# Kernel tuning notes

Hardware: AMD Instinct MI355X
Metric: run time of the kernel (lower is better)

Reference implementation:

```python
import jax, jax.numpy as jnp
import numpy as np

E = 1024
H = 16
DFF = 4 * E
EPS = 1e-5


def layer_norm(x, scale, bias):
    mu = jnp.mean(x, axis=-1, keepdims=True)
    var = jnp.var(x, axis=-1, keepdims=True)
    return (x - mu) * jax.lax.rsqrt(var + EPS) * scale + bias


def setup_inputs() -> dict:
    key = jax.random.key(0)
    ks = jax.random.split(key, 12)
    N, L = 2, 2048
    x = jax.random.normal(ks[0], (N, L, E), dtype=jnp.float32)
    attn_mask = jax.random.randint(ks[1], (N, H, L, L), 0, 2) == 1
    s = 0.02
    return {
        "x": x,
        "attn_mask": attn_mask,
        "ln1_s": jnp.ones((E,), jnp.float32),
        "ln1_b": jnp.zeros((E,), jnp.float32),
        "Wqkv": jax.random.normal(ks[2], (E, 3 * E), jnp.float32) * s,
        "bqkv": jnp.zeros((3 * E,), jnp.float32),
        "Wo": jax.random.normal(ks[3], (E, E), jnp.float32) * s,
        "bo": jnp.zeros((E,), jnp.float32),
        "ln2_s": jnp.ones((E,), jnp.float32),
        "ln2_b": jnp.zeros((E,), jnp.float32),
        "lnf_s": jnp.ones((E,), jnp.float32),
        "lnf_b": jnp.zeros((E,), jnp.float32),
        "W1": jax.random.normal(ks[4], (E, DFF), jnp.float32) * s,
        "b1": jnp.zeros((DFF,), jnp.float32),
        "W2": jax.random.normal(ks[5], (DFF, E), jnp.float32) * s,
        "b2": jnp.zeros((E,), jnp.float32),
    }


def reference(x, attn_mask, ln1_s, ln1_b, Wqkv, bqkv, Wo, bo,
              ln2_s, ln2_b, lnf_s, lnf_b, W1, b1, W2, b2):
    N, L, _ = x.shape
    D = E // H
    # --- self attention (pre-norm) ---
    h = layer_norm(x, ln1_s, ln1_b)
    qkv = h @ Wqkv + bqkv                      # [N,L,3E]
    q, k, v = jnp.split(qkv, 3, axis=-1)
    q = q.reshape(N, L, H, D)
    k = k.reshape(N, L, H, D)
    v = v.reshape(N, L, H, D)
    a = jnp.einsum('nqhd,nkhd->nhqk', q, k) * (D ** -0.5)  # [N,H,L,L]
    a = jnp.where(attn_mask, -jnp.inf, a)
    a = jax.nn.softmax(a, axis=-1)
    o = jnp.einsum('nhqk,nkhd->nqhd', a, v).reshape(N, L, E)
    o = o @ Wo + bo
    x = x + o
    # --- feedforward (norm_2 then FF's internal LN) ---
    h = layer_norm(x, ln2_s, ln2_b)
    h = layer_norm(h, lnf_s, lnf_b)
    h = jax.nn.gelu(h @ W1 + b1, approximate=False) @ W2 + b2
    return x + h
```

## Files before the change

kernel.cpp:

```cpp
#include <hip/hip_runtime.h>
#include <math.h>

#define E_DIM 1024
#define H_HEADS 16
#define D_HEAD 64
#define DFF_DIM 4096
#define L_SEQ 2048
#define N_BATCH 2
#define T_TOK (N_BATCH * L_SEQ)

typedef __attribute__((ext_vector_type(8))) __bf16 bf16x8;
typedef __attribute__((ext_vector_type(4))) float f32x4;

__device__ __forceinline__ unsigned short f2bf(float f) {
  union { float f; unsigned int u; } v; v.f = f;
  unsigned int r = v.u + 0x7fffu + ((v.u >> 16) & 1u);
  return (unsigned short)(r >> 16);
}

__global__ __launch_bounds__(256) void convert_transpose(
    const float* __restrict__ in, unsigned short* __restrict__ out, int K, int N) {
  __shared__ float tile[32][33];
  int n0 = blockIdx.x * 32, k0 = blockIdx.y * 32;
  int tx = threadIdx.x & 31, ty = threadIdx.x >> 5;
#pragma unroll
  for (int i = 0; i < 32; i += 8)
    tile[ty + i][tx] = in[(size_t)(k0 + ty + i) * N + n0 + tx];
  __syncthreads();
#pragma unroll
  for (int i = 0; i < 32; i += 8)
    out[(size_t)(n0 + ty + i) * K + k0 + tx] = f2bf(tile[tx][ty + i]);
}

__device__ __forceinline__ void block_reduce2(float& a, float& b, float* sm, int tid) {
#pragma unroll
  for (int off = 32; off > 0; off >>= 1) {
    a += __shfl_down(a, off);
    b += __shfl_down(b, off);
  }
  int wid = tid >> 6;
  if ((tid & 63) == 0) { sm[wid * 2] = a; sm[wid * 2 + 1] = b; }
  __syncthreads();
  a = sm[0] + sm[2] + sm[4] + sm[6];
  b = sm[1] + sm[3] + sm[5] + sm[7];
}

__global__ __launch_bounds__(256) void ln_kernel(
    const float* __restrict__ x, const float* __restrict__ s,
    const float* __restrict__ b, unsigned short* __restrict__ out) {
  int row = blockIdx.x, tid = threadIdx.x;
  __shared__ float sm[8];
  float4 v = ((const float4*)(x + (size_t)row * E_DIM))[tid];
  float sum = v.x + v.y + v.z + v.w;
  float sq = v.x * v.x + v.y * v.y + v.z * v.z + v.w * v.w;
  block_reduce2(sum, sq, sm, tid);
  float mu = sum * (1.0f / E_DIM);
  float var = sq * (1.0f / E_DIM) - mu * mu;
  float rs = rsqrtf(var + 1e-5f);
  float4 sv = ((const float4*)s)[tid];
  float4 bv = ((const float4*)b)[tid];
  ushort4 o4;
  o4.x = f2bf((v.x - mu) * rs * sv.x + bv.x);
  o4.y = f2bf((v.y - mu) * rs * sv.y + bv.y);
  o4.z = f2bf((v.z - mu) * rs * sv.z + bv.z);
  o4.w = f2bf((v.w - mu) * rs * sv.w + bv.w);
  ((ushort4*)(out + (size_t)row * E_DIM))[tid] = o4;
}

__global__ __launch_bounds__(256) void ln2_kernel(
    const float* __restrict__ x, const float* __restrict__ s2,
    const float* __restrict__ b2, const float* __restrict__ sf,
    const float* __restrict__ bf_, unsigned short* __restrict__ out) {
  int row = blockIdx.x, tid = threadIdx.x;
  __shared__ float sm[8];
  float4 v = ((const float4*)(x + (size_t)row * E_DIM))[tid];
  float sum = v.x + v.y + v.z + v.w;
  float sq = v.x * v.x + v.y * v.y + v.z * v.z + v.w * v.w;
  block_reduce2(sum, sq, sm, tid);
  float mu = sum * (1.0f / E_DIM);
  float rs = rsqrtf(sq * (1.0f / E_DIM) - mu * mu + 1e-5f);
  float4 s2v = ((const float4*)s2)[tid];
  float4 b2v = ((const float4*)b2)[tid];
  float y0 = (v.x - mu) * rs * s2v.x + b2v.x;
  float y1 = (v.y - mu) * rs * s2v.y + b2v.y;
  float y2 = (v.z - mu) * rs * s2v.z + b2v.z;
  float y3 = (v.w - mu) * rs * s2v.w + b2v.w;
  float sum2 = y0 + y1 + y2 + y3;
  float sq2 = y0 * y0 + y1 * y1 + y2 * y2 + y3 * y3;
  __syncthreads();
  block_reduce2(sum2, sq2, sm, tid);
  float mu2 = sum2 * (1.0f / E_DIM);
  float rs2 = rsqrtf(sq2 * (1.0f / E_DIM) - mu2 * mu2 + 1e-5f);
  float4 sfv = ((const float4*)sf)[tid];
  float4 bfv = ((const float4*)bf_)[tid];
  ushort4 o4;
  o4.x = f2bf((y0 - mu2) * rs2 * sfv.x + bfv.x);
  o4.y = f2bf((y1 - mu2) * rs2 * sfv.y + bfv.y);
  o4.z = f2bf((y2 - mu2) * rs2 * sfv.z + bfv.z);
  o4.w = f2bf((y3 - mu2) * rs2 * sfv.w + bfv.w);
  ((ushort4*)(out + (size_t)row * E_DIM))[tid] = o4;
}

template <int EPI>
__global__ __launch_bounds__(256) void gemm_bt(
    const unsigned short* __restrict__ A, const unsigned short* __restrict__ Bt,
    const float* __restrict__ bias, const float* __restrict__ resid,
    void* __restrict__ outp, int M, int N, int K) {
  __shared__ unsigned short As[128 * 40];
  __shared__ unsigned short Bs[128 * 40];
  int tid = threadIdx.x;
  int lane = tid & 63, wave = tid >> 6;
  int m0 = blockIdx.y * 128, n0 = blockIdx.x * 128;
  int wm = (wave & 1) * 64, wn = (wave >> 1) * 64;
  int lm = lane & 15, lq = lane >> 4;
  int trow = tid >> 2, tcol = tid & 3;
  f32x4 acc[4][4] = {};
  for (int k0 = 0; k0 < K; k0 += 32) {
    uint4 av0 = *(const uint4*)(A + (size_t)(m0 + trow) * K + k0 + tcol * 8);
    uint4 av1 = *(const uint4*)(A + (size_t)(m0 + trow + 64) * K + k0 + tcol * 8);
    uint4 bv0 = *(const uint4*)(Bt + (size_t)(n0 + trow) * K + k0 + tcol * 8);
    uint4 bv1 = *(const uint4*)(Bt + (size_t)(n0 + trow + 64) * K + k0 + tcol * 8);
    __syncthreads();
    *(uint4*)(As + trow * 40 + tcol * 8) = av0;
    *(uint4*)(As + (trow + 64) * 40 + tcol * 8) = av1;
    *(uint4*)(Bs + trow * 40 + tcol * 8) = bv0;
    *(uint4*)(Bs + (trow + 64) * 40 + tcol * 8) = bv1;
    __syncthreads();
    bf16x8 a[4], b[4];
#pragma unroll
    for (int i = 0; i < 4; i++)
      a[i] = *(const bf16x8*)(As + (wm + i * 16 + lm) * 40 + lq * 8);
#pragma unroll
    for (int j = 0; j < 4; j++)
      b[j] = *(const bf16x8*)(Bs + (wn + j * 16 + lm) * 40 + lq * 8);
#pragma unroll
    for (int i = 0; i < 4; i++)
#pragma unroll
      for (int j = 0; j < 4; j++)
        acc[i][j] = __builtin_amdgcn_mfma_f32_16x16x32_bf16(a[i], b[j], acc[i][j], 0, 0, 0);
  }
#pragma unroll
  for (int i = 0; i < 4; i++)
#pragma unroll
    for (int j = 0; j < 4; j++) {
      int row = m0 + wm + i * 16 + lq * 4;
      int col = n0 + wn + j * 16 + lm;
      float bcol = bias[col];
#pragma unroll
      for (int r = 0; r < 4; r++) {
        float v = acc[i][j][r] + bcol;
        size_t idx = (size_t)(row + r) * N + col;
        if (EPI == 0) {
          ((unsigned short*)outp)[idx] = f2bf(v);
        } else if (EPI == 1) {
          float g = 0.5f * v * (1.0f + erff(v * 0.70710678118f));
          ((unsigned short*)outp)[idx] = f2bf(g);
        } else {
          ((float*)outp)[idx] = resid[idx] + v;
        }
      }
    }
}

__global__ __launch_bounds__(256) void attn_kernel(
    const unsigned short* __restrict__ qkv, const int* __restrict__ mask,
    unsigned short* __restrict__ o) {
  const int bq = blockIdx.x;
  const int nh = blockIdx.y;
  const int h = nh & 15;
  const int tid = threadIdx.x, lane = tid & 63, wave = tid >> 6;
  const int lm = lane & 15, lq = lane >> 4;

  __shared__ unsigned short Ks[64 * 72];
  __shared__ unsigned short Vs[64 * 66];
  __shared__ unsigned short Ps[4][16 * 72];

  const int q_base = bq * 64;
  const int tok0 = (nh >> 4) * L_SEQ;
  const int qoff = h * 64, koff = E_DIM + h * 64, voff = 2 * E_DIM + h * 64;
  const int* mbase = mask + (size_t)nh * L_SEQ * L_SEQ;

  bf16x8 qf[2];
  {
    int t = tok0 + q_base + wave * 16 + lm;
    const unsigned short* qr = qkv + (size_t)t * (3 * E_DIM) + qoff + lq * 8;
    qf[0] = *(const bf16x8*)(qr);
    qf[1] = *(const bf16x8*)(qr + 32);
  }

  float m_run[4], l_run[4];
  f32x4 oacc[4] = {};
#pragma unroll
  for (int r = 0; r < 4; r++) { m_run[r] = -1e30f; l_run[r] = 0.0f; }

  for (int kt = 0; kt < L_SEQ / 64; kt++) {
    const int k_base = kt * 64;
    __syncthreads();
    {
      int row = tid >> 3, chunk = tid & 7;
#pragma unroll
      for (int it = 0; it < 2; it++) {
        int key = row + it * 32;
        int t = tok0 + k_base + key;
        uint4 kv = *(const uint4*)(qkv + (size_t)t * (3 * E_DIM) + koff + chunk * 8);
        *(uint4*)(Ks + key * 72 + chunk * 8) = kv;
        uint4 vv = *(const uint4*)(qkv + (size_t)t * (3 * E_DIM) + voff + chunk * 8);
        unsigned int* vw = (unsigned int*)(Vs + key * 66 + chunk * 8);
        vw[0] = vv.x; vw[1] = vv.y; vw[2] = vv.z; vw[3] = vv.w;
      }
    }
    __syncthreads();

    f32x4 s[4];
#pragma unroll
    for (int nt = 0; nt < 4; nt++) {
      bf16x8 kb0 = *(const bf16x8*)(Ks + (nt * 16 + lm) * 72 + lq * 8);
      bf16x8 kb1 = *(const bf16x8*)(Ks + (nt * 16 + lm) * 72 + 32 + lq * 8);
      f32x4 acc = {};
      acc = __builtin_amdgcn_mfma_f32_16x16x32_bf16(qf[0], kb0, acc, 0, 0, 0);
      acc = __builtin_amdgcn_mfma_f32_16x16x32_bf16(qf[1], kb1, acc, 0, 0, 0);
      s[nt] = acc;
    }
    const int qrow = q_base + wave * 16 + lq * 4;
#pragma unroll
    for (int nt = 0; nt < 4; nt++) {
      int kcol = k_base + nt * 16 + lm;
#pragma unroll
      for (int r = 0; r < 4; r++) {
        float v = s[nt][r] * 0.125f;
        int mval = mbase[(size_t)(qrow + r) * L_SEQ + kcol];
        s[nt][r] = mval ? -1e30f : v;
      }
    }
    float alpha[4], rsum[4];
#pragma unroll
    for (int r = 0; r < 4; r++) {
      float v = fmaxf(fmaxf(s[0][r], s[1][r]), fmaxf(s[2][r], s[3][r]));
#pragma unroll
      for (int mo = 1; mo < 16; mo <<= 1) v = fmaxf(v, __shfl_xor(v, mo));
      float mn = fmaxf(m_run[r], v);
      alpha[r] = __expf(m_run[r] - mn);
      m_run[r] = mn;
      rsum[r] = 0.0f;
    }
    unsigned short* pw = Ps[wave];
#pragma unroll
    for (int nt = 0; nt < 4; nt++)
#pragma unroll
      for (int r = 0; r < 4; r++) {
        float p = __expf(s[nt][r] - m_run[r]);
        rsum[r] += p;
        pw[(lq * 4 + r) * 72 + nt * 16 + lm] = f2bf(p);
      }
#pragma unroll
    for (int r = 0; r < 4; r++) {
      float v = rsum[r];
#pragma unroll
      for (int mo = 1; mo < 16; mo <<= 1) v += __shfl_xor(v, mo);
      l_run[r] = l_run[r] * alpha[r] + v;
    }
#pragma unroll
    for (int j = 0; j < 4; j++)
#pragma unroll
      for (int r = 0; r < 4; r++) oacc[j][r] *= alpha[r];
    __syncthreads();

#pragma unroll
    for (int c = 0; c < 2; c++) {
      bf16x8 pa = *(const bf16x8*)(pw + lm * 72 + c * 32 + lq * 8);
#pragma unroll
      for (int j = 0; j < 4; j++) {
        bf16x8 vb;
#pragma unroll
        for (int jj = 0; jj < 8; jj++)
          vb[jj] = *(const __bf16*)(Vs + (c * 32 + lq * 8 + jj) * 66 + j * 16 + lm);
        oacc[j] = __builtin_amdgcn_mfma_f32_16x16x32_bf16(pa, vb, oacc[j], 0, 0, 0);
      }
    }
  }
  const int qrow = q_base + wave * 16 + lq * 4;
#pragma unroll
  for (int r = 0; r < 4; r++) {
    float inv_l = 1.0f / l_run[r];
    int t = tok0 + qrow + r;
#pragma unroll
    for (int j = 0; j < 4; j++)
      o[(size_t)t * E_DIM + h * 64 + j * 16 + lm] = f2bf(oacc[j][r] * inv_l);
  }
}

extern "C" void kernel_launch(void* const* d_in, const int* in_sizes, int n_in,
                              void* d_out, int out_size, void* d_ws, size_t ws_size,
                              hipStream_t stream) {
  const float* x = (const float*)d_in[0];
  const int* mask = (const int*)d_in[1];
  const float* ln1_s = (const float*)d_in[2];
  const float* ln1_b = (const float*)d_in[3];
  const float* Wqkv = (const float*)d_in[4];
  const float* bqkv = (const float*)d_in[5];
  const float* Wo = (const float*)d_in[6];
  const float* bo = (const float*)d_in[7];
  const float* ln2_s = (const float*)d_in[8];
  const float* ln2_b = (const float*)d_in[9];
  const float* lnf_s = (const float*)d_in[10];
  const float* lnf_b = (const float*)d_in[11];
  const float* W1 = (const float*)d_in[12];
  const float* b1 = (const float*)d_in[13];
  const float* W2 = (const float*)d_in[14];
  const float* b2 = (const float*)d_in[15];

  size_t off = 0;
  auto alloc = [&](size_t bytes) {
    void* p = (char*)d_ws + off;
    off += (bytes + 255) & ~(size_t)255;
    return p;
  };
  unsigned short* WqkvT = (unsigned short*)alloc((size_t)3072 * 1024 * 2);
  unsigned short* WoT = (unsigned short*)alloc((size_t)1024 * 1024 * 2);
  unsigned short* W1T = (unsigned short*)alloc((size_t)4096 * 1024 * 2);
  unsigned short* W2T = (unsigned short*)alloc((size_t)1024 * 4096 * 2);
  unsigned short* h1 = (unsigned short*)alloc((size_t)T_TOK * E_DIM * 2);
  unsigned short* qkvb = (unsigned short*)alloc((size_t)T_TOK * 3 * E_DIM * 2);
  unsigned short* ob = (unsigned short*)alloc((size_t)T_TOK * E_DIM * 2);
  float* x2 = (float*)alloc((size_t)T_TOK * E_DIM * 4);
  unsigned short* h2 = (unsigned short*)alloc((size_t)T_TOK * E_DIM * 2);
  unsigned short* g1 = (unsigned short*)alloc((size_t)T_TOK * DFF_DIM * 2);

  convert_transpose<<<dim3(3072 / 32, 1024 / 32), 256, 0, stream>>>(Wqkv, WqkvT, 1024, 3072);
  convert_transpose<<<dim3(1024 / 32, 1024 / 32), 256, 0, stream>>>(Wo, WoT, 1024, 1024);
  convert_transpose<<<dim3(4096 / 32, 1024 / 32), 256, 0, stream>>>(W1, W1T, 1024, 4096);
  convert_transpose<<<dim3(1024 / 32, 4096 / 32), 256, 0, stream>>>(W2, W2T, 4096, 1024);
  ln_kernel<<<T_TOK, 256, 0, stream>>>(x, ln1_s, ln1_b, h1);
  gemm_bt<0><<<dim3(3072 / 128, T_TOK / 128), 256, 0, stream>>>(
      h1, WqkvT, bqkv, nullptr, qkvb, T_TOK, 3072, 1024);
  attn_kernel<<<dim3(L_SEQ / 64, N_BATCH * H_HEADS), 256, 0, stream>>>(qkvb, mask, ob);
  gemm_bt<2><<<dim3(1024 / 128, T_TOK / 128), 256, 0, stream>>>(
      ob, WoT, bo, x, x2, T_TOK, 1024, 1024);
  ln2_kernel<<<T_TOK, 256, 0, stream>>>(x2, ln2_s, ln2_b, lnf_s, lnf_b, h2);
  gemm_bt<1><<<dim3(DFF_DIM / 128, T_TOK / 128), 256, 0, stream>>>(
      h2, W1T, b1, nullptr, g1, T_TOK, DFF_DIM, 1024);
  gemm_bt<2><<<dim3(1024 / 128, T_TOK / 128), 256, 0, stream>>>(
      g1, W2T, b2, x2, (float*)d_out, T_TOK, 1024, 4096);

  (void)in_sizes; (void)n_in; (void)out_size; (void)ws_size;
}
```

Before: 1.071 ms.

## Load GEMM tiles directly into LDS and store V transposed with XOR swizzle

The GEMM mainloop now uses global_load_lds to copy A and B tiles straight from global memory into LDS, skipping the register round-trip, and drops the padding from the LDS layout. The attention kernel stores V transposed into LDS with an XOR swizzle, so each PV MFMA operand is fetched with one 16-byte read instead of eight scalar bf16 reads. The unpadded GEMM LDS layout may bring back bank conflicts on fragment reads, and the transposed V store becomes eight scalar LDS writes per chunk.

```diff
diff --git a/kernel.cpp b/kernel.cpp
--- a/kernel.cpp
+++ b/kernel.cpp
@@ -16,6 +16,12 @@
   union { float f; unsigned int u; } v; v.f = f;
   unsigned int r = v.u + 0x7fffu + ((v.u >> 16) & 1u);
   return (unsigned short)(r >> 16);
+}
+
+__device__ __forceinline__ void gld16(const void* g, void* l) {
+  __builtin_amdgcn_global_load_lds(
+      (const __attribute__((address_space(1))) unsigned int*)g,
+      (__attribute__((address_space(3))) unsigned int*)l, 16, 0, 0);
 }
 
 __global__ __launch_bounds__(256) void convert_transpose(
@@ -106,33 +112,34 @@
     const unsigned short* __restrict__ A, const unsigned short* __restrict__ Bt,
     const float* __restrict__ bias, const float* __restrict__ resid,
     void* __restrict__ outp, int M, int N, int K) {
-  __shared__ unsigned short As[128 * 40];
-  __shared__ unsigned short Bs[128 * 40];
+  __shared__ unsigned short As[128 * 32];
+  __shared__ unsigned short Bs[128 * 32];
   int tid = threadIdx.x;
   int lane = tid & 63, wave = tid >> 6;
   int m0 = blockIdx.y * 128, n0 = blockIdx.x * 128;
   int wm = (wave & 1) * 64, wn = (wave >> 1) * 64;
   int lm = lane & 15, lq = lane >> 4;
-  int trow = tid >> 2, tcol = tid & 3;
+  int srow = wave * 32 + (lane >> 2);
+  int scol = (lane & 3) * 8;
+  const unsigned short* Ag = A + (size_t)(m0 + srow) * K + scol;
+  const unsigned short* Bg = Bt + (size_t)(n0 + srow) * K + scol;
+  unsigned short* AsW = As + wave * 1024;
+  unsigned short* BsW = Bs + wave * 1024;
   f32x4 acc[4][4] = {};
   for (int k0 = 0; k0 < K; k0 += 32) {
-    uint4 av0 = *(const uint4*)(A + (size_t)(m0 + trow) * K + k0 + tcol * 8);
-    uint4 av1 = *(const uint4*)(A + (size_t)(m0 + trow + 64) * K + k0 + tcol * 8);
-    uint4 bv0 = *(const uint4*)(Bt + (size_t)(n0 + trow) * K + k0 + tcol * 8);
-    uint4 bv1 = *(const uint4*)(Bt + (size_t)(n0 + trow + 64) * K + k0 + tcol * 8);
-    __syncthreads();
-    *(uint4*)(As + trow * 40 + tcol * 8) = av0;
-    *(uint4*)(As + (trow + 64) * 40 + tcol * 8) = av1;
-    *(uint4*)(Bs + trow * 40 + tcol * 8) = bv0;
-    *(uint4*)(Bs + (trow + 64) * 40 + tcol * 8) = bv1;
+    __syncthreads();
+    gld16(Ag + k0, AsW);
+    gld16(Ag + (size_t)16 * K + k0, AsW + 512);
+    gld16(Bg + k0, BsW);
+    gld16(Bg + (size_t)16 * K + k0, BsW + 512);
     __syncthreads();
     bf16x8 a[4], b[4];
 #pragma unroll
     for (int i = 0; i < 4; i++)
-      a[i] = *(const bf16x8*)(As + (wm + i * 16 + lm) * 40 + lq * 8);
+      a[i] = *(const bf16x8*)(As + (wm + i * 16 + lm) * 32 + lq * 8);
 #pragma unroll
     for (int j = 0; j < 4; j++)
-      b[j] = *(const bf16x8*)(Bs + (wn + j * 16 + lm) * 40 + lq * 8);
+      b[j] = *(const bf16x8*)(Bs + (wn + j * 16 + lm) * 32 + lq * 8);
 #pragma unroll
     for (int i = 0; i < 4; i++)
 #pragma unroll
@@ -172,7 +179,7 @@
   const int lm = lane & 15, lq = lane >> 4;
 
   __shared__ unsigned short Ks[64 * 72];
-  __shared__ unsigned short Vs[64 * 66];
+  __shared__ unsigned short Vt[64 * 72];
   __shared__ unsigned short Ps[4][16 * 72];
 
   const int q_base = bq * 64;
@@ -205,8 +212,11 @@
         uint4 kv = *(const uint4*)(qkv + (size_t)t * (3 * E_DIM) + koff + chunk * 8);
         *(uint4*)(Ks + key * 72 + chunk * 8) = kv;
         uint4 vv = *(const uint4*)(qkv + (size_t)t * (3 * E_DIM) + voff + chunk * 8);
-        unsigned int* vw = (unsigned int*)(Vs + key * 66 + chunk * 8);
-        vw[0] = vv.x; vw[1] = vv.y; vw[2] = vv.z; vw[3] = vv.w;
+        const unsigned short* vs = (const unsigned short*)&vv;
+        int kcol = key ^ (chunk << 3);
+#pragma unroll
+        for (int jj = 0; jj < 8; jj++)
+          Vt[(chunk * 8 + jj) * 72 + kcol] = vs[jj];
       }
     }
     __syncthreads();
@@ -270,10 +280,9 @@
       bf16x8 pa = *(const bf16x8*)(pw + lm * 72 + c * 32 + lq * 8);
 #pragma unroll
       for (int j = 0; j < 4; j++) {
-        bf16x8 vb;
-#pragma unroll
-        for (int jj = 0; jj < 8; jj++)
-          vb[jj] = *(const __bf16*)(Vs + (c * 32 + lq * 8 + jj) * 66 + j * 16 + lm);
+        int d = j * 16 + lm;
+        int kblk = (c * 4 + lq) ^ ((d >> 3) & 7);
+        bf16x8 vb = *(const bf16x8*)(Vt + d * 72 + kblk * 8);
         oacc[j] = __builtin_amdgcn_mfma_f32_16x16x32_bf16(pa, vb, oacc[j], 0, 0, 0);
       }
     }
```

Result: no change. 1.081 ms (+0.9%).
